# Optimization experiments

Measured on AMD Instinct MI355X. Metric: run time of the kernel, lower is better.

Reference implementation:

```python
import jax, jax.numpy as jnp
import numpy as np
import math

B, C, H, W = 4, 256, 56, 56
RC = 32  # max(256 // 8, 8)
EPS = 1e-5


def _conv(x, w, pad):
    return jax.lax.conv_general_dilated(
        x, w, window_strides=(1, 1), padding=[(pad, pad), (pad, pad)],
        dimension_numbers=('NCHW', 'OIHW', 'NCHW'))


def setup_inputs() -> dict:
    key = jax.random.key(0)
    ks = jax.random.split(key, 9)
    s = 0.05  # keep attention logits in a sane range
    return {
        'x': jax.random.normal(ks[0], (B, C, H, W), jnp.float32),
        'wq1': jax.random.normal(ks[1], (RC, C, 1, 1), jnp.float32) * s,
        'wq3': jax.random.normal(ks[2], (RC, C, 3, 3), jnp.float32) * s,
        'wq5': jax.random.normal(ks[3], (RC, C, 5, 5), jnp.float32) * s,
        'wq7': jax.random.normal(ks[4], (RC, C, 7, 7), jnp.float32) * s,
        'wk': jax.random.normal(ks[5], (RC, C, 1, 1), jnp.float32) * s,
        'wv': jax.random.normal(ks[6], (C, C, 1, 1), jnp.float32) * s,
        'wproj': jax.random.normal(ks[7], (C, 4 * C, 1, 1), jnp.float32) * s,
        'gamma': jnp.ones((C,), jnp.float32),
        'beta': jnp.zeros((C,), jnp.float32),
    }


def reference(x, wq1, wq3, wq5, wq7, wk, wv, wproj, gamma, beta):
    b, c, h, w = x.shape
    hw = h * w
    scale = 1.0 / math.sqrt(RC)
    k = _conv(x, wk, 0).reshape(b, RC, hw)   # [B, RC, HW]
    v = _conv(x, wv, 0).reshape(b, c, hw)    # [B, C, HW]
    attended = []
    for wq, pad in ((wq1, 0), (wq3, 1), (wq5, 2), (wq7, 3)):
        q = _conv(x, wq, pad).reshape(b, RC, hw)          # [B, RC, HW]
        scores = jnp.einsum('bri,brj->bij', q, k) * scale  # [B, HW, HW]
        attn = jax.nn.softmax(scores, axis=-1)
        att = jnp.einsum('bcj,bij->bci', v, attn)          # [B, C, HW]
        attended.append(att.reshape(b, c, h, w))
    concat = jnp.concatenate(attended, axis=1)             # [B, 4C, H, W]
    out = _conv(concat, wproj, 0) + x                      # residual before BN
    # BatchNorm2d in training mode: batch stats (biased var), affine
    mean = out.mean(axis=(0, 2, 3), keepdims=True)
    var = out.var(axis=(0, 2, 3), keepdims=True)
    out = (out - mean) * jax.lax.rsqrt(var + EPS)
    return out * gamma[None, :, None, None] + beta[None, :, None, None]
```

## Files before the change

kernel.cpp:

```cpp
#include <hip/hip_runtime.h>
#include <hip/hip_bf16.h>
#include <math.h>

#define HW 3136
#define WIDTH 56
#define CC 256
#define BB 4
#define RCH 32
#define SCLOG2E 0.2550437041556575f

using bf16x8 = __attribute__((ext_vector_type(8))) short;
using f32x4  = __attribute__((ext_vector_type(4))) float;

static __device__ __forceinline__ unsigned short f2bf(float f) {
    __hip_bfloat16 h = __float2bfloat16(f);
    return *reinterpret_cast<unsigned short*>(&h);
}

__global__ __launch_bounds__(256) void gemm1x1_v(
    const float* __restrict__ in, const float* __restrict__ w,
    unsigned short* __restrict__ out, int Cin, int Cout) {
    const int tx = threadIdx.x & 15;
    const int ty = threadIdx.x >> 4;
    const int i0 = blockIdx.y * 64;
    const int co0 = blockIdx.x * 16;
    const int b = blockIdx.z;

    __shared__ float xs[32][64];
    __shared__ float wsl[16][33];

    float acc[4] = {0.f, 0.f, 0.f, 0.f};
    const float* inb = in + (size_t)b * Cin * HW;

    for (int c0 = 0; c0 < Cin; c0 += 32) {
        #pragma unroll
        for (int k = 0; k < 8; ++k) {
            int e = threadIdx.x + k * 256;
            int r = e >> 6, col = e & 63;
            xs[r][col] = inb[(size_t)(c0 + r) * HW + i0 + col];
        }
        #pragma unroll
        for (int k = 0; k < 2; ++k) {
            int e = threadIdx.x + k * 256;
            int r = e >> 5, col = e & 31;
            wsl[r][col] = w[(size_t)(co0 + r) * Cin + c0 + col];
        }
        __syncthreads();
        #pragma unroll
        for (int c = 0; c < 32; ++c) {
            float wv = wsl[ty][c];
            #pragma unroll
            for (int u = 0; u < 4; ++u)
                acc[u] += wv * xs[c][tx + 16 * u];
        }
        __syncthreads();
    }

    size_t obase = ((size_t)b * Cout + co0 + ty) * HW + i0 + tx;
    #pragma unroll
    for (int u = 0; u < 4; ++u)
        out[obase + 16 * u] = f2bf(acc[u]);
}

__global__ __launch_bounds__(256) void gemm_qk32(
    const float* __restrict__ in, const float* __restrict__ w,
    unsigned short* __restrict__ outt, float oscale) {
    const int i = threadIdx.x & 63;
    const int cog = threadIdx.x >> 6;
    const int i0 = blockIdx.x * 64;
    const int b = blockIdx.y;

    __shared__ float xs[32][64];
    __shared__ float wsl[32][33];

    float acc[8] = {0.f,0.f,0.f,0.f,0.f,0.f,0.f,0.f};
    const float* inb = in + (size_t)b * CC * HW;

    for (int c0 = 0; c0 < CC; c0 += 32) {
        #pragma unroll
        for (int k = 0; k < 8; ++k) {
            int e = threadIdx.x + k * 256;
            int r = e >> 6, col = e & 63;
            xs[r][col] = inb[(size_t)(c0 + r) * HW + i0 + col];
        }
        #pragma unroll
        for (int k = 0; k < 4; ++k) {
            int e = threadIdx.x + k * 256;
            int r = e >> 5, col = e & 31;
            wsl[r][col] = w[(size_t)r * CC + c0 + col];
        }
        __syncthreads();
        #pragma unroll
        for (int c = 0; c < 32; ++c) {
            float xv = xs[c][i];
            #pragma unroll
            for (int u = 0; u < 8; ++u)
                acc[u] += wsl[cog * 8 + u][c] * xv;
        }
        __syncthreads();
    }
    unsigned int pk[4];
    #pragma unroll
    for (int u = 0; u < 4; ++u)
        pk[u] = (unsigned int)f2bf(acc[2 * u] * oscale) |
                ((unsigned int)f2bf(acc[2 * u + 1] * oscale) << 16);
    *(uint4*)(outt + ((size_t)b * HW + i0 + i) * 32 + cog * 8) = *(uint4*)pk;
}

__global__ __launch_bounds__(256) void transpose_x(
    const float* __restrict__ x, unsigned short* __restrict__ xT) {
    __shared__ unsigned short tile[32][33];
    const int b = blockIdx.z;
    const int i0 = blockIdx.x * 32, c0 = blockIdx.y * 32;
    const int tx = threadIdx.x & 31, ty = threadIdx.x >> 5;
    #pragma unroll
    for (int k = 0; k < 4; ++k)
        tile[ty + k * 8][tx] = f2bf(x[((size_t)b * CC + c0 + ty + k * 8) * HW + i0 + tx]);
    __syncthreads();
    #pragma unroll
    for (int k = 0; k < 4; ++k)
        xT[((size_t)b * HW + i0 + ty + k * 8) * 256 + c0 + tx] = tile[tx][ty + k * 8];
}

__global__ __launch_bounds__(256) void wprep(
    const float* __restrict__ w, unsigned short* __restrict__ Wb, int KT) {
    int e = blockIdx.x * 256 + threadIdx.x;
    if (e < KT * 32 * 256) {
        int c = e & 255, r = (e >> 8) & 31, t = e >> 13;
        Wb[e] = f2bf(w[((size_t)r * 256 + c) * KT + t]);
    }
}

__global__ __launch_bounds__(256) void cvt_bf16(
    const float* __restrict__ src, unsigned short* __restrict__ dst, int n) {
    int e = blockIdx.x * 256 + threadIdx.x;
    if (e < n) dst[e] = f2bf(src[e]);
}

template <int KS>
static __device__ __forceinline__ void qconv_body(
    const unsigned short* __restrict__ xT,
    const unsigned short* __restrict__ Wb,
    unsigned short* __restrict__ q,
    unsigned short (*xs)[40]) {
    constexpr int P = (KS - 1) / 2;
    constexpr int KT = KS * KS;
    constexpr int ROWS = 64 + 114 * P;
    const int b = blockIdx.y;
    const int i0 = blockIdx.x * 64;
    const int t = threadIdx.x;
    const int lane = t & 63;
    const int w = t >> 6;
    const int li = lane & 15;
    const int lg = lane >> 4;

    const int base = i0 - P * 57;
    const int mycol = (i0 + w * 16 + li) % WIDTH;

    f32x4 acc[2];
    acc[0] = (f32x4){0.f, 0.f, 0.f, 0.f};
    acc[1] = (f32x4){0.f, 0.f, 0.f, 0.f};

    const unsigned short* xTb = xT + (size_t)b * HW * 256;

    for (int c0 = 0; c0 < 256; c0 += 32) {
        __syncthreads();
        for (int e = t; e < ROWS * 4; e += 256) {
            int row = e >> 2, cs = e & 3;
            int gidx = base + row;
            uint4 val = make_uint4(0, 0, 0, 0);
            if (gidx >= 0 && gidx < HW)
                val = *(const uint4*)(xTb + (size_t)gidx * 256 + c0 + cs * 8);
            *(uint4*)(&xs[row][cs * 8]) = val;
        }
        __syncthreads();

        #pragma unroll
        for (int tap = 0; tap < KT; ++tap) {
            const int dx = tap % KS - P;
            const int poff = (tap / KS) * WIDTH + tap % KS;
            bf16x8 a = *(const bf16x8*)(&xs[w * 16 + li + poff][lg * 8]);
            if ((unsigned)(mycol + dx) >= (unsigned)WIDTH)
                a = (bf16x8){0, 0, 0, 0, 0, 0, 0, 0};
            const unsigned short* wrow =
                Wb + (size_t)tap * 32 * 256 + c0 + lg * 8;
            bf16x8 b0 = *(const bf16x8*)(wrow + (size_t)li * 256);
            bf16x8 b1 = *(const bf16x8*)(wrow + (size_t)(16 + li) * 256);
            acc[0] = __builtin_amdgcn_mfma_f32_16x16x32_bf16(a, b0, acc[0], 0, 0, 0);
            acc[1] = __builtin_amdgcn_mfma_f32_16x16x32_bf16(a, b1, acc[1], 0, 0, 0);
        }
    }

    unsigned short* qb = q + ((size_t)b * HW + i0 + w * 16 + lg * 4) * 32;
    #pragma unroll
    for (int rs = 0; rs < 2; ++rs)
        #pragma unroll
        for (int r = 0; r < 4; ++r)
            qb[(size_t)r * 32 + rs * 16 + li] = f2bf(acc[rs][r] * SCLOG2E);
}

__global__ __launch_bounds__(256) void qconv_all(
    const unsigned short* __restrict__ xT,
    const unsigned short* __restrict__ Wb3,
    const unsigned short* __restrict__ Wb5,
    const unsigned short* __restrict__ Wb7,
    unsigned short* __restrict__ Qt) {
    __shared__ unsigned short xs[406][40];
    const size_t QSLICE = (size_t)BB * HW * 32;
    if (blockIdx.z == 0)      qconv_body<3>(xT, Wb3, Qt + 1 * QSLICE, xs);
    else if (blockIdx.z == 1) qconv_body<5>(xT, Wb5, Qt + 2 * QSLICE, xs);
    else                      qconv_body<7>(xT, Wb7, Qt + 3 * QSLICE, xs);
}

__global__ __launch_bounds__(256) void flashmfma(
    const unsigned short* __restrict__ Qt, const unsigned short* __restrict__ Kt,
    const unsigned short* __restrict__ Vb, unsigned short* __restrict__ ATTb) {
    const int b = blockIdx.y, g = blockIdx.z;
    const int i0 = blockIdx.x * 64;
    const int t = threadIdx.x;
    const int lane = t & 63;
    const int w = t >> 6;
    const int lg = lane >> 4;
    const int li = lane & 15;

    __shared__ __align__(16) unsigned short Ps[64][72];
    __shared__ float lls[64];

    const bf16x8 aq = *(const bf16x8*)(
        Qt + ((size_t)(g * BB + b) * HW + i0 + w * 16 + li) * 32 + lg * 8);

    const f32x4 z4 = (f32x4){0.f, 0.f, 0.f, 0.f};
    f32x4 acc[4][4];
    #pragma unroll
    for (int ct = 0; ct < 4; ++ct)
        #pragma unroll
        for (int is = 0; is < 4; ++is) acc[ct][is] = z4;

    float lsum[4] = {0.f, 0.f, 0.f, 0.f};

    const unsigned short* Kb = Kt + (size_t)b * HW * 32;
    const unsigned short* Vw = Vb + ((size_t)b * CC + w * 64) * HW;

    for (int jt = 0; jt < HW / 64; ++jt) {
        const int j0 = jt * 64;

        f32x4 S[4];
        #pragma unroll
        for (int j2 = 0; j2 < 4; ++j2) {
            bf16x8 bk = *(const bf16x8*)(Kb + (size_t)(j0 + j2 * 16 + li) * 32 + lg * 8);
            S[j2] = __builtin_amdgcn_mfma_f32_16x16x32_bf16(aq, bk, z4, 0, 0, 0);
        }

        unsigned int pk0[4], pk1[4];
        #pragma unroll
        for (int r = 0; r < 4; ++r) {
            float p0 = __builtin_amdgcn_exp2f(S[0][r]);
            float p1 = __builtin_amdgcn_exp2f(S[1][r]);
            float p2 = __builtin_amdgcn_exp2f(S[2][r]);
            float p3 = __builtin_amdgcn_exp2f(S[3][r]);
            lsum[r] += (p0 + p1) + (p2 + p3);
            asm("v_cvt_pk_bf16_f32 %0, %1, %2" : "=v"(pk0[r]) : "v"(p0), "v"(p1));
            asm("v_cvt_pk_bf16_f32 %0, %1, %2" : "=v"(pk1[r]) : "v"(p2), "v"(p3));
        }

        __syncthreads();
        #pragma unroll
        for (int r = 0; r < 4; ++r) {
            const int row = w * 16 + lg * 4 + r;
            Ps[row][li]      = (unsigned short)pk0[r];
            Ps[row][16 + li] = (unsigned short)(pk0[r] >> 16);
            Ps[row][32 + li] = (unsigned short)pk1[r];
            Ps[row][48 + li] = (unsigned short)(pk1[r] >> 16);
        }
        __syncthreads();

        bf16x8 bp[4][2];
        #pragma unroll
        for (int is = 0; is < 4; ++is)
            #pragma unroll
            for (int ks = 0; ks < 2; ++ks)
                bp[is][ks] = *(const bf16x8*)(&Ps[is * 16 + li][ks * 32 + lg * 8]);

        #pragma unroll
        for (int ct = 0; ct < 4; ++ct) {
            #pragma unroll
            for (int ks = 0; ks < 2; ++ks) {
                bf16x8 av = *(const bf16x8*)(
                    Vw + (size_t)(ct * 16 + li) * HW + j0 + ks * 32 + lg * 8);
                #pragma unroll
                for (int is = 0; is < 4; ++is)
                    acc[ct][is] = __builtin_amdgcn_mfma_f32_16x16x32_bf16(
                        av, bp[is][ks], acc[ct][is], 0, 0, 0);
            }
        }
    }

    #pragma unroll
    for (int r = 0; r < 4; ++r) {
        float s = lsum[r];
        #pragma unroll
        for (int off = 1; off < 16; off <<= 1) s += __shfl_xor(s, off);
        if (li == 0) lls[w * 16 + lg * 4 + r] = s;
    }
    __syncthreads();

    float invl[4];
    #pragma unroll
    for (int is = 0; is < 4; ++is) invl[is] = 1.f / lls[is * 16 + li];

    #pragma unroll
    for (int ct = 0; ct < 4; ++ct)
        #pragma unroll
        for (int is = 0; is < 4; ++is)
            #pragma unroll
            for (int r = 0; r < 4; ++r) {
                int c = w * 64 + ct * 16 + lg * 4 + r;
                ATTb[((size_t)b * (4 * CC) + g * CC + c) * HW + i0 + is * 16 + li] =
                    f2bf(acc[ct][is][r] * invl[is]);
            }
}

__global__ __launch_bounds__(256) void gemm_proj(
    const unsigned short* __restrict__ ATTb, const unsigned short* __restrict__ Wpb,
    const float* __restrict__ x, float* __restrict__ out) {
    const int b = blockIdx.y;
    const int i0 = blockIdx.x * 32;
    const int t = threadIdx.x;
    const int lane = t & 63;
    const int w = t >> 6;
    const int lg = lane >> 4;
    const int li = lane & 15;

    __shared__ __align__(16) unsigned short As[32][72];

    const f32x4 z4 = (f32x4){0.f, 0.f, 0.f, 0.f};
    f32x4 acc[4][2];
    #pragma unroll
    for (int ct = 0; ct < 4; ++ct) { acc[ct][0] = z4; acc[ct][1] = z4; }

    for (int k0 = 0; k0 < 1024; k0 += 64) {
        __syncthreads();
        {
            int row = t >> 2, seg = t & 3;
            uint4 v = *(const uint4*)(
                ATTb + ((size_t)b * 1024 + k0 + row) * HW + i0 + seg * 8);
            const unsigned short* sv = (const unsigned short*)&v;
            #pragma unroll
            for (int u = 0; u < 8; ++u) As[seg * 8 + u][row] = sv[u];
        }
        __syncthreads();

        #pragma unroll
        for (int k2 = 0; k2 < 2; ++k2) {
            bf16x8 afr[2];
            #pragma unroll
            for (int is = 0; is < 2; ++is)
                afr[is] = *(const bf16x8*)(&As[is * 16 + li][k2 * 32 + lg * 8]);
            #pragma unroll
            for (int ct = 0; ct < 4; ++ct) {
                bf16x8 wf = *(const bf16x8*)(
                    Wpb + (size_t)(w * 64 + ct * 16 + li) * 1024 + k0 + k2 * 32 + lg * 8);
                #pragma unroll
                for (int is = 0; is < 2; ++is)
                    acc[ct][is] = __builtin_amdgcn_mfma_f32_16x16x32_bf16(
                        wf, afr[is], acc[ct][is], 0, 0, 0);
            }
        }
    }

    #pragma unroll
    for (int ct = 0; ct < 4; ++ct)
        #pragma unroll
        for (int is = 0; is < 2; ++is)
            #pragma unroll
            for (int r = 0; r < 4; ++r) {
                int co = w * 64 + ct * 16 + lg * 4 + r;
                size_t o = ((size_t)b * CC + co) * HW + i0 + is * 16 + li;
                out[o] = acc[ct][is][r] + x[o];
            }
}

__global__ __launch_bounds__(256) void bnstats(
    const float* __restrict__ out, float* __restrict__ mean,
    float* __restrict__ rstd) {
    const int c = blockIdx.x;
    float s = 0.f, s2 = 0.f;
    for (int e = threadIdx.x; e < BB * HW; e += 256) {
        int b = e / HW, i = e - b * HW;
        float v = out[((size_t)b * CC + c) * HW + i];
        s += v; s2 += v * v;
    }
    __shared__ float rs[256], rs2[256];
    rs[threadIdx.x] = s; rs2[threadIdx.x] = s2;
    __syncthreads();
    for (int st = 128; st > 0; st >>= 1) {
        if (threadIdx.x < st) {
            rs[threadIdx.x] += rs[threadIdx.x + st];
            rs2[threadIdx.x] += rs2[threadIdx.x + st];
        }
        __syncthreads();
    }
    if (threadIdx.x == 0) {
        const float n = (float)(BB * HW);
        float m = rs[0] / n;
        float var = rs2[0] / n - m * m;
        mean[c] = m;
        rstd[c] = rsqrtf(var + 1e-5f);
    }
}

__global__ __launch_bounds__(256) void bnapply(
    float* __restrict__ out, const float* __restrict__ mean,
    const float* __restrict__ rstd, const float* __restrict__ gamma,
    const float* __restrict__ beta) {
    size_t idx = (size_t)blockIdx.x * 256 + threadIdx.x;
    if (idx < (size_t)BB * CC * HW) {
        int c = (int)((idx / HW) % CC);
        out[idx] = (out[idx] - mean[c]) * rstd[c] * gamma[c] + beta[c];
    }
}

extern "C" void kernel_launch(void* const* d_in, const int* in_sizes, int n_in,
                              void* d_out, int out_size, void* d_ws, size_t ws_size,
                              hipStream_t stream) {
    const float* x     = (const float*)d_in[0];
    const float* wq1   = (const float*)d_in[1];
    const float* wq3   = (const float*)d_in[2];
    const float* wq5   = (const float*)d_in[3];
    const float* wq7   = (const float*)d_in[4];
    const float* wk    = (const float*)d_in[5];
    const float* wv    = (const float*)d_in[6];
    const float* wproj = (const float*)d_in[7];
    const float* gamma = (const float*)d_in[8];
    const float* beta  = (const float*)d_in[9];
    float* out = (float*)d_out;

    unsigned short* ATTb = (unsigned short*)d_ws;
    unsigned short* Kt   = ATTb + (size_t)BB * 4 * CC * HW;
    unsigned short* Qt   = Kt + (size_t)BB * HW * 32;
    unsigned short* Vb   = Qt + (size_t)4 * BB * HW * 32;
    unsigned short* xT   = Vb + (size_t)BB * CC * HW;
    unsigned short* Wb3  = xT + (size_t)BB * HW * CC;
    unsigned short* Wb5  = Wb3 + (size_t)9 * 32 * 256;
    unsigned short* Wb7  = Wb5 + (size_t)25 * 32 * 256;
    unsigned short* Wpb  = Wb7 + (size_t)49 * 32 * 256;
    float* mean = (float*)(Wpb + (size_t)256 * 1024);
    float* rstd = mean + CC;

    dim3 blk(256);

    wprep<<<dim3((9 * 8192 + 255) / 256), blk, 0, stream>>>(wq3, Wb3, 9);
    wprep<<<dim3((25 * 8192 + 255) / 256), blk, 0, stream>>>(wq5, Wb5, 25);
    wprep<<<dim3((49 * 8192 + 255) / 256), blk, 0, stream>>>(wq7, Wb7, 49);
    cvt_bf16<<<dim3((256 * 1024 + 255) / 256), blk, 0, stream>>>(wproj, Wpb, 256 * 1024);
    transpose_x<<<dim3(HW / 32, CC / 32, BB), blk, 0, stream>>>(x, xT);

    gemm_qk32<<<dim3(HW / 64, BB), blk, 0, stream>>>(x, wk, Kt, 1.0f);
    gemm_qk32<<<dim3(HW / 64, BB), blk, 0, stream>>>(x, wq1, Qt, SCLOG2E);
    gemm1x1_v<<<dim3(CC / 16, HW / 64, BB), blk, 0, stream>>>(x, wv, Vb, CC, CC);

    qconv_all<<<dim3(HW / 64, BB, 3), blk, 0, stream>>>(xT, Wb3, Wb5, Wb7, Qt);

    flashmfma<<<dim3(HW / 64, BB, 4), blk, 0, stream>>>(Qt, Kt, Vb, ATTb);

    gemm_proj<<<dim3(HW / 32, BB), blk, 0, stream>>>(ATTb, Wpb, x, out);

    bnstats<<<dim3(CC), blk, 0, stream>>>(out, mean, rstd);
    bnapply<<<dim3((BB * CC * HW + 255) / 256), blk, 0, stream>>>(out, mean, rstd, gamma, beta);
}
```

Baseline: 582.5 us.

## Compute K, Q1 and V projections with bf16 MFMA and fuse weight prep

Replaces the scalar fp32 shared-memory GEMMs for the K, Q1 and V 1x1 projections with bf16 MFMA kernels that read the already-transposed bf16 x. K and Q1 now run in one launch split over a grid z dimension. All weight conversion kernels are merged into a single prep_weights launch that also converts wk, wq1 and wv to bf16. This cuts launch count and the FP32 ALU cost of the projections, at the price of bf16 rounding of the x and weight inputs to those projections.

```diff
diff --git a/kernel.cpp b/kernel.cpp
--- a/kernel.cpp
+++ b/kernel.cpp
@@ -7,6 +7,7 @@
 #define CC 256
 #define BB 4
 #define RCH 32
+#define NJT (HW / 64)
 #define SCLOG2E 0.2550437041556575f
 
 using bf16x8 = __attribute__((ext_vector_type(8))) short;
@@ -17,94 +18,36 @@
     return *reinterpret_cast<unsigned short*>(&h);
 }
 
-__global__ __launch_bounds__(256) void gemm1x1_v(
-    const float* __restrict__ in, const float* __restrict__ w,
-    unsigned short* __restrict__ out, int Cin, int Cout) {
-    const int tx = threadIdx.x & 15;
-    const int ty = threadIdx.x >> 4;
-    const int i0 = blockIdx.y * 64;
-    const int co0 = blockIdx.x * 16;
-    const int b = blockIdx.z;
-
-    __shared__ float xs[32][64];
-    __shared__ float wsl[16][33];
-
-    float acc[4] = {0.f, 0.f, 0.f, 0.f};
-    const float* inb = in + (size_t)b * Cin * HW;
-
-    for (int c0 = 0; c0 < Cin; c0 += 32) {
-        #pragma unroll
-        for (int k = 0; k < 8; ++k) {
-            int e = threadIdx.x + k * 256;
-            int r = e >> 6, col = e & 63;
-            xs[r][col] = inb[(size_t)(c0 + r) * HW + i0 + col];
-        }
-        #pragma unroll
-        for (int k = 0; k < 2; ++k) {
-            int e = threadIdx.x + k * 256;
-            int r = e >> 5, col = e & 31;
-            wsl[r][col] = w[(size_t)(co0 + r) * Cin + c0 + col];
-        }
-        __syncthreads();
-        #pragma unroll
-        for (int c = 0; c < 32; ++c) {
-            float wv = wsl[ty][c];
-            #pragma unroll
-            for (int u = 0; u < 4; ++u)
-                acc[u] += wv * xs[c][tx + 16 * u];
-        }
-        __syncthreads();
-    }
-
-    size_t obase = ((size_t)b * Cout + co0 + ty) * HW + i0 + tx;
-    #pragma unroll
-    for (int u = 0; u < 4; ++u)
-        out[obase + 16 * u] = f2bf(acc[u]);
-}
-
-__global__ __launch_bounds__(256) void gemm_qk32(
-    const float* __restrict__ in, const float* __restrict__ w,
-    unsigned short* __restrict__ outt, float oscale) {
-    const int i = threadIdx.x & 63;
-    const int cog = threadIdx.x >> 6;
-    const int i0 = blockIdx.x * 64;
-    const int b = blockIdx.y;
-
-    __shared__ float xs[32][64];
-    __shared__ float wsl[32][33];
-
-    float acc[8] = {0.f,0.f,0.f,0.f,0.f,0.f,0.f,0.f};
-    const float* inb = in + (size_t)b * CC * HW;
-
-    for (int c0 = 0; c0 < CC; c0 += 32) {
-        #pragma unroll
-        for (int k = 0; k < 8; ++k) {
-            int e = threadIdx.x + k * 256;
-            int r = e >> 6, col = e & 63;
-            xs[r][col] = inb[(size_t)(c0 + r) * HW + i0 + col];
-        }
-        #pragma unroll
-        for (int k = 0; k < 4; ++k) {
-            int e = threadIdx.x + k * 256;
-            int r = e >> 5, col = e & 31;
-            wsl[r][col] = w[(size_t)r * CC + c0 + col];
-        }
-        __syncthreads();
-        #pragma unroll
-        for (int c = 0; c < 32; ++c) {
-            float xv = xs[c][i];
-            #pragma unroll
-            for (int u = 0; u < 8; ++u)
-                acc[u] += wsl[cog * 8 + u][c] * xv;
-        }
-        __syncthreads();
-    }
-    unsigned int pk[4];
-    #pragma unroll
-    for (int u = 0; u < 4; ++u)
-        pk[u] = (unsigned int)f2bf(acc[2 * u] * oscale) |
-                ((unsigned int)f2bf(acc[2 * u + 1] * oscale) << 16);
-    *(uint4*)(outt + ((size_t)b * HW + i0 + i) * 32 + cog * 8) = *(uint4*)pk;
+__global__ __launch_bounds__(256) void prep_weights(
+    const float* __restrict__ wq3, const float* __restrict__ wq5,
+    const float* __restrict__ wq7, const float* __restrict__ wproj,
+    const float* __restrict__ wk, const float* __restrict__ wq1,
+    const float* __restrict__ wv,
+    unsigned short* __restrict__ Wb3, unsigned short* __restrict__ Wb5,
+    unsigned short* __restrict__ Wb7, unsigned short* __restrict__ Wpb,
+    unsigned short* __restrict__ Wkq, unsigned short* __restrict__ Wvb) {
+    int e = blockIdx.x * 256 + threadIdx.x;
+    if (e < 73728) {
+        int c = e & 255, r = (e >> 8) & 31, t = e >> 13;
+        Wb3[e] = f2bf(wq3[((size_t)r * 256 + c) * 9 + t]);
+    } else if (e < 278528) {
+        int i = e - 73728;
+        int c = i & 255, r = (i >> 8) & 31, t = i >> 13;
+        Wb5[i] = f2bf(wq5[((size_t)r * 256 + c) * 25 + t]);
+    } else if (e < 679936) {
+        int i = e - 278528;
+        int c = i & 255, r = (i >> 8) & 31, t = i >> 13;
+        Wb7[i] = f2bf(wq7[((size_t)r * 256 + c) * 49 + t]);
+    } else if (e < 942080) {
+        int i = e - 679936;
+        Wpb[i] = f2bf(wproj[i]);
+    } else if (e < 958464) {
+        int i = e - 942080;
+        Wkq[i] = f2bf(i < 8192 ? wk[i] : wq1[i - 8192]);
+    } else if (e < 1024000) {
+        int i = e - 958464;
+        Wvb[i] = f2bf(wv[i]);
+    }
 }
 
 __global__ __launch_bounds__(256) void transpose_x(
@@ -122,19 +65,76 @@
         xT[((size_t)b * HW + i0 + ty + k * 8) * 256 + c0 + tx] = tile[tx][ty + k * 8];
 }
 
-__global__ __launch_bounds__(256) void wprep(
-    const float* __restrict__ w, unsigned short* __restrict__ Wb, int KT) {
-    int e = blockIdx.x * 256 + threadIdx.x;
-    if (e < KT * 32 * 256) {
-        int c = e & 255, r = (e >> 8) & 31, t = e >> 13;
-        Wb[e] = f2bf(w[((size_t)r * 256 + c) * KT + t]);
-    }
-}
-
-__global__ __launch_bounds__(256) void cvt_bf16(
-    const float* __restrict__ src, unsigned short* __restrict__ dst, int n) {
-    int e = blockIdx.x * 256 + threadIdx.x;
-    if (e < n) dst[e] = f2bf(src[e]);
+__global__ __launch_bounds__(256) void qk32_mfma(
+    const unsigned short* __restrict__ xT, const unsigned short* __restrict__ Wkq,
+    unsigned short* __restrict__ Kt, unsigned short* __restrict__ Qt) {
+    const int b = blockIdx.y, z = blockIdx.z;
+    const int i0 = blockIdx.x * 64;
+    const int t = threadIdx.x;
+    const int lane = t & 63, w = t >> 6, lg = lane >> 4, li = lane & 15;
+
+    unsigned short* outp = z == 0 ? Kt : Qt;
+    const float osc = z == 0 ? 1.0f : SCLOG2E;
+    const unsigned short* wb = Wkq + z * 8192;
+    const unsigned short* xb = xT + ((size_t)b * HW + i0 + w * 16 + li) * 256;
+
+    const f32x4 z4 = (f32x4){0.f, 0.f, 0.f, 0.f};
+    f32x4 acc[2] = {z4, z4};
+
+    for (int c0 = 0; c0 < 256; c0 += 32) {
+        bf16x8 ax = *(const bf16x8*)(xb + c0 + lg * 8);
+        #pragma unroll
+        for (int rs = 0; rs < 2; ++rs) {
+            bf16x8 bw = *(const bf16x8*)(wb + (size_t)(rs * 16 + li) * 256 + c0 + lg * 8);
+            acc[rs] = __builtin_amdgcn_mfma_f32_16x16x32_bf16(ax, bw, acc[rs], 0, 0, 0);
+        }
+    }
+    unsigned short* qb = outp + ((size_t)b * HW + i0 + w * 16 + lg * 4) * 32;
+    #pragma unroll
+    for (int rs = 0; rs < 2; ++rs)
+        #pragma unroll
+        for (int r = 0; r < 4; ++r)
+            qb[(size_t)r * 32 + rs * 16 + li] = f2bf(acc[rs][r] * osc);
+}
+
+__global__ __launch_bounds__(256) void v_mfma(
+    const unsigned short* __restrict__ xT, const unsigned short* __restrict__ Wvb,
+    unsigned short* __restrict__ Vb) {
+    const int b = blockIdx.y;
+    const int i0 = blockIdx.x * 32;
+    const int t = threadIdx.x;
+    const int lane = t & 63, w = t >> 6, lg = lane >> 4, li = lane & 15;
+
+    const f32x4 z4 = (f32x4){0.f, 0.f, 0.f, 0.f};
+    f32x4 acc[4][2];
+    #pragma unroll
+    for (int ct = 0; ct < 4; ++ct) { acc[ct][0] = z4; acc[ct][1] = z4; }
+
+    const unsigned short* xb = xT + (size_t)b * HW * 256;
+
+    for (int c0 = 0; c0 < 256; c0 += 32) {
+        bf16x8 bx[2];
+        #pragma unroll
+        for (int is = 0; is < 2; ++is)
+            bx[is] = *(const bf16x8*)(xb + (size_t)(i0 + is * 16 + li) * 256 + c0 + lg * 8);
+        #pragma unroll
+        for (int ct = 0; ct < 4; ++ct) {
+            bf16x8 aw = *(const bf16x8*)(
+                Wvb + (size_t)(w * 64 + ct * 16 + li) * 256 + c0 + lg * 8);
+            #pragma unroll
+            for (int is = 0; is < 2; ++is)
+                acc[ct][is] = __builtin_amdgcn_mfma_f32_16x16x32_bf16(
+                    aw, bx[is], acc[ct][is], 0, 0, 0);
+        }
+    }
+    #pragma unroll
+    for (int ct = 0; ct < 4; ++ct)
+        #pragma unroll
+        for (int is = 0; is < 2; ++is)
+            #pragma unroll
+            for (int r = 0; r < 4; ++r)
+                Vb[((size_t)b * CC + w * 64 + ct * 16 + lg * 4 + r) * HW +
+                   i0 + is * 16 + li] = f2bf(acc[ct][is][r]);
 }
 
 template <int KS>
@@ -241,7 +241,7 @@
     const unsigned short* Kb = Kt + (size_t)b * HW * 32;
     const unsigned short* Vw = Vb + ((size_t)b * CC + w * 64) * HW;
 
-    for (int jt = 0; jt < HW / 64; ++jt) {
+    for (int jt = 0; jt < NJT; ++jt) {
         const int j0 = jt * 64;
 
         f32x4 S[4];
@@ -444,20 +444,19 @@
     unsigned short* Wb5  = Wb3 + (size_t)9 * 32 * 256;
     unsigned short* Wb7  = Wb5 + (size_t)25 * 32 * 256;
     unsigned short* Wpb  = Wb7 + (size_t)49 * 32 * 256;
-    float* mean = (float*)(Wpb + (size_t)256 * 1024);
+    unsigned short* Wkq  = Wpb + (size_t)256 * 1024;
+    unsigned short* Wvb  = Wkq + (size_t)2 * 32 * 256;
+    float* mean = (float*)(Wvb + (size_t)256 * 256);
     float* rstd = mean + CC;
 
     dim3 blk(256);
 
-    wprep<<<dim3((9 * 8192 + 255) / 256), blk, 0, stream>>>(wq3, Wb3, 9);
-    wprep<<<dim3((25 * 8192 + 255) / 256), blk, 0, stream>>>(wq5, Wb5, 25);
-    wprep<<<dim3((49 * 8192 + 255) / 256), blk, 0, stream>>>(wq7, Wb7, 49);
-    cvt_bf16<<<dim3((256 * 1024 + 255) / 256), blk, 0, stream>>>(wproj, Wpb, 256 * 1024);
+    prep_weights<<<dim3(4000), blk, 0, stream>>>(
+        wq3, wq5, wq7, wproj, wk, wq1, wv, Wb3, Wb5, Wb7, Wpb, Wkq, Wvb);
     transpose_x<<<dim3(HW / 32, CC / 32, BB), blk, 0, stream>>>(x, xT);
 
-    gemm_qk32<<<dim3(HW / 64, BB), blk, 0, stream>>>(x, wk, Kt, 1.0f);
-    gemm_qk32<<<dim3(HW / 64, BB), blk, 0, stream>>>(x, wq1, Qt, SCLOG2E);
-    gemm1x1_v<<<dim3(CC / 16, HW / 64, BB), blk, 0, stream>>>(x, wv, Vb, CC, CC);
+    qk32_mfma<<<dim3(HW / 64, BB, 2), blk, 0, stream>>>(xT, Wkq, Kt, Qt);
+    v_mfma<<<dim3(HW / 32, BB), blk, 0, stream>>>(xT, Wvb, Vb);
 
     qconv_all<<<dim3(HW / 64, BB, 3), blk, 0, stream>>>(xT, Wb3, Wb5, Wb7, Qt);
 
```

After: 494.8 us. 1.18x faster.
